# Performance work log

Hardware: AMD Instinct MI355X
Metric: run time of the kernel (lower is better)

Reference implementation:

```python
import jax, jax.numpy as jnp
import numpy as np

EPS = 1e-5  # torch LayerNorm default
NUM_HEADS = 8


def layernorm(x, g, b):
    m = jnp.mean(x, axis=-1, keepdims=True)
    v = jnp.var(x, axis=-1, keepdims=True)
    return (x - m) * jax.lax.rsqrt(v + EPS) * g + b


def dwconv(x_img, w, b):
    # x_img: [B,C,H,W]; w: [C,1,k,k] depthwise, 'same' padding
    C = x_img.shape[1]
    k = w.shape[-1]
    out = jax.lax.conv_general_dilated(
        x_img, w, (1, 1), [(k // 2, k // 2)] * 2,
        dimension_numbers=('NCHW', 'OIHW', 'NCHW'), feature_group_count=C)
    return out + b[None, :, None, None]


def _forward(x, domain_label, cpe_w, cpe_b, ln1_g, ln1_b, qkv_w, proj_w, proj_b,
             dl_w1, dl_b1, dl_w2, dl_b2, crpe_w3, crpe_b3, crpe_w5, crpe_b5,
             crpe_w7, crpe_b7, ln2_g, ln2_b, fc1_w, fc1_b, fc2_w, fc2_b, H, W, d):
    B, N, C = x.shape
    h = NUM_HEADS
    Ch = C // h
    scale = Ch ** (-0.5)

    # ---- CPE: depthwise 3x3 conv positional encoding with residual ----
    xi = x.transpose(0, 2, 1).reshape(B, C, H, W)
    xi = dwconv(xi, cpe_w, cpe_b) + xi
    x = xi.reshape(B, C, N).transpose(0, 2, 1)

    # ---- domain-indexed LayerNorm 1 (d is a static python int) ----
    cur = layernorm(x, ln1_g[d], ln1_b[d])

    # ---- factorized attention ----
    qkv = (cur @ qkv_w).reshape(B, N, 3, h, Ch).transpose(2, 0, 3, 1, 4)
    q, k, v = qkv[0], qkv[1], qkv[2]          # each [B,h,N,Ch]
    k_sm = jax.nn.softmax(k, axis=2)          # softmax over tokens
    kv = jnp.einsum('bhnk,bhnv->bhkv', k_sm, v)       # [B,h,Ch,Ch]
    factor_att = jnp.einsum('bhnk,bhkv->bhnv', q, kv)  # [B,h,N,Ch]

    # ---- conv relative position encoding (window splits {3:2,5:3,7:3}) ----
    v_img = v.transpose(0, 1, 3, 2).reshape(B, C, H, W)
    g1 = dwconv(v_img[:, :2 * Ch], crpe_w3, crpe_b3)
    g2 = dwconv(v_img[:, 2 * Ch:5 * Ch], crpe_w5, crpe_b5)
    g3 = dwconv(v_img[:, 5 * Ch:], crpe_w7, crpe_b7)
    conv_v = jnp.concatenate([g1, g2, g3], axis=1)        # [B,C,H,W]
    conv_v = conv_v.reshape(B, h, Ch, N).transpose(0, 1, 3, 2)
    crpe = q * conv_v                                      # [B,h,N,Ch]

    factor_att = scale * factor_att + crpe

    # ---- per-domain softmax gating over heads ----
    da = jax.nn.relu(domain_label @ dl_w1 + dl_b1) @ dl_w2 + dl_b2  # [B, h*Ch]
    da = da.reshape(B, h, Ch)[:, :, None, :]                        # [B,h,1,Ch]
    da = jax.nn.softmax(da, axis=1)                                  # over heads
    attn = (da * factor_att).transpose(0, 2, 1, 3).reshape(B, N, C)
    attn = attn @ proj_w + proj_b

    x = x + attn

    # ---- domain-indexed LayerNorm 2 + MLP ----
    cur = layernorm(x, ln2_g[d], ln2_b[d])
    cur = jax.nn.gelu(cur @ fc1_w + fc1_b, approximate=False) @ fc2_w + fc2_b
    return x + cur


def setup_inputs() -> dict:
    key = jax.random.key(0)
    ks = iter(jax.random.split(key, 32))
    B, H, W, C, h, nd = 8, 56, 56, 256, 8, 4
    N = H * W
    Ch = C // h
    hid = C // 2   # domain MLP hidden = max(dim//r,4), r=2
    mh = 4 * C     # mlp_ratio=4
    r = lambda shape, s=0.02: jax.random.normal(next(ks), shape, jnp.float32) * s
    return dict(
        x=jax.random.normal(next(ks), (B, N, C), jnp.float32),
        domain_label=jax.nn.one_hot(
            jax.random.randint(next(ks), (B,), 0, nd), nd, dtype=jnp.float32),
        cpe_w=r((C, 1, 3, 3)), cpe_b=jnp.zeros((C,), jnp.float32),
        ln1_g=jnp.ones((nd, C), jnp.float32), ln1_b=jnp.zeros((nd, C), jnp.float32),
        qkv_w=r((C, 3 * C)),
        proj_w=r((C, C)), proj_b=jnp.zeros((C,), jnp.float32),
        dl_w1=r((nd, hid)), dl_b1=jnp.zeros((hid,), jnp.float32),
        dl_w2=r((hid, C)), dl_b2=jnp.zeros((C,), jnp.float32),
        crpe_w3=r((2 * Ch, 1, 3, 3)), crpe_b3=jnp.zeros((2 * Ch,), jnp.float32),
        crpe_w5=r((3 * Ch, 1, 5, 5)), crpe_b5=jnp.zeros((3 * Ch,), jnp.float32),
        crpe_w7=r((3 * Ch, 1, 7, 7)), crpe_b7=jnp.zeros((3 * Ch,), jnp.float32),
        ln2_g=jnp.ones((nd, C), jnp.float32), ln2_b=jnp.zeros((nd, C), jnp.float32),
        fc1_w=r((C, mh)), fc1_b=jnp.zeros((mh,), jnp.float32),
        fc2_w=r((mh, C)), fc2_b=jnp.zeros((C,), jnp.float32),
        H=H, W=W, d=0,
    )


def reference(x, domain_label, cpe_w, cpe_b, ln1_g, ln1_b, qkv_w, proj_w, proj_b,
              dl_w1, dl_b1, dl_w2, dl_b2, crpe_w3, crpe_b3, crpe_w5, crpe_b5,
              crpe_w7, crpe_b7, ln2_g, ln2_b, fc1_w, fc1_b, fc2_w, fc2_b, H, W, d):
    return _forward(x, domain_label, cpe_w, cpe_b, ln1_g, ln1_b, qkv_w, proj_w,
                    proj_b, dl_w1, dl_b1, dl_w2, dl_b2, crpe_w3, crpe_b3, crpe_w5,
                    crpe_b5, crpe_w7, crpe_b7, ln2_g, ln2_b, fc1_w, fc1_b, fc2_w,
                    fc2_b, H, W, d)
```

## Files before the change

### kernel.cpp

```cpp
#include <hip/hip_runtime.h>
#include <hip/hip_bf16.h>
#include <math.h>

#define BB 8
#define HH 56
#define WW 56
#define NN (HH*WW)
#define CC 256
#define NH 8
#define NT (BB*NN)
#define HID 128
#define MH 1024
#define SCALE 0.17677669529663687f

typedef __attribute__((ext_vector_type(8))) short bf16x8;
typedef __attribute__((ext_vector_type(4))) float f32x4;

__device__ __forceinline__ ushort f2bf(float f) {
    __hip_bfloat16 h = __float2bfloat16(f);
    return *(ushort*)&h;
}
__device__ __forceinline__ float bf2f(ushort u) {
    union { unsigned int i; float f; } x; x.i = ((unsigned int)u) << 16; return x.f;
}
__device__ __forceinline__ uint pk2(float lo, float hi) {
    return ((uint)f2bf(hi) << 16) | (uint)f2bf(lo);
}
__device__ __forceinline__ float unlo(uint u) { return __uint_as_float(u << 16); }
__device__ __forceinline__ float unhi(uint u) { return __uint_as_float(u & 0xFFFF0000u); }

__device__ __forceinline__ void gload16(const void* g, void* s) {
    __builtin_amdgcn_global_load_lds(
        (const __attribute__((address_space(1))) void*)g,
        (__attribute__((address_space(3))) void*)s, 16, 0, 0);
}

__global__ __launch_bounds__(256) void wtrans_kernel(
    const float* __restrict__ w, ushort* __restrict__ wt, int K, int N)
{
    __shared__ float tile[32][33];
    const int t = threadIdx.x;
    const int col = t & 31, rw = t >> 5;
    const int k0 = blockIdx.y * 32, n0 = blockIdx.x * 32;
    #pragma unroll
    for (int i = rw; i < 32; i += 8)
        tile[i][col] = w[(size_t)(k0 + i) * N + n0 + col];
    __syncthreads();
    #pragma unroll
    for (int i = rw; i < 32; i += 8) {
        int n = n0 + i;
        int nl = n & 63;
        int np = (n & ~63) | ((nl & 3) * 16 + (nl >> 2));
        wt[(size_t)np * K + k0 + col] = f2bf(tile[col][i]);
    }
}

__global__ __launch_bounds__(256) void wpack_kernel(
    const float* __restrict__ w3, const float* __restrict__ b3,
    const float* __restrict__ w5, const float* __restrict__ b5,
    const float* __restrict__ w7, const float* __restrict__ b7,
    uint* __restrict__ wt, float* __restrict__ bt)
{
    const int qq = blockIdx.x;
    const int KSQ = (qq == 0) ? 3 : (qq == 1) ? 5 : 7;
    for (int idx = threadIdx.x; idx < 49 * 32; idx += 256) {
        int tap = idx >> 5, p = idx & 31;
        int cA = qq * 64 + 2 * p;
        float lo = 0.f, hi = 0.f;
        if (tap < KSQ * KSQ) {
            int dy = tap / KSQ, dx = tap - dy * KSQ;
            const float* wb; int kslo;
            if (cA < 64)       { wb = w3 + cA * 9;          kslo = 3; }
            else if (cA < 160) { wb = w5 + (cA - 64) * 25;  kslo = 5; }
            else               { wb = w7 + (cA - 160) * 49; kslo = 7; }
            int offp = KSQ / 2 - kslo / 2;
            int sy = dy - offp, sx = dx - offp;
            if (sy >= 0 && sy < kslo && sx >= 0 && sx < kslo) {
                lo = wb[sy * kslo + sx];
                hi = wb[kslo * kslo + sy * kslo + sx];
            }
        }
        wt[(qq * 49 + tap) * 32 + p] = pk2(lo, hi);
    }
    if (threadIdx.x < 32) {
        int p = threadIdx.x, cA = qq * 64 + 2 * p;
        float blo, bhi;
        if (cA < 64)       { blo = b3[cA];       bhi = b3[cA + 1]; }
        else if (cA < 160) { blo = b5[cA - 64];  bhi = b5[cA - 63]; }
        else               { blo = b7[cA - 160]; bhi = b7[cA - 159]; }
        bt[(qq * 32 + p) * 2]     = blo;
        bt[(qq * 32 + p) * 2 + 1] = bhi;
    }
}

__global__ __launch_bounds__(256) void cpack_kernel(
    const float* __restrict__ w, const float* __restrict__ bias,
    uint* __restrict__ wt, float* __restrict__ bt)
{
    const int qq = blockIdx.x;
    for (int idx = threadIdx.x; idx < 9 * 32; idx += 256) {
        int tap = idx >> 5, p = idx & 31;
        int cA = qq * 64 + 2 * p;
        wt[(qq * 9 + tap) * 32 + p] = pk2(w[cA * 9 + tap], w[(cA + 1) * 9 + tap]);
    }
    if (threadIdx.x < 32) {
        int p = threadIdx.x, cA = qq * 64 + 2 * p;
        bt[(qq * 32 + p) * 2]     = bias[cA];
        bt[(qq * 32 + p) * 2 + 1] = bias[cA + 1];
    }
}

__global__ __launch_bounds__(256) void cpe_kernel(
    const float* __restrict__ x, const uint* __restrict__ wtab,
    const float* __restrict__ btab, float* __restrict__ out)
{
    __shared__ uint vt[4 * 34 * 32];
    const int qq = blockIdx.x >> 1, hx = blockIdx.x & 1;
    const int y0 = blockIdx.y * 2, b = blockIdx.z;
    const int x0 = hx * 28;
    const int t = threadIdx.x;
    const int c0 = qq * 64;
    const int p = t & 31;

    uint wpk[9];
    #pragma unroll
    for (int i = 0; i < 9; ++i) wpk[i] = wtab[(qq * 9 + i) * 32 + p];
    const float2 bb = *(const float2*)(btab + (qq * 32 + p) * 2);

    for (int pos = t >> 5; pos < 4 * 34; pos += 8) {
        int row = pos / 34, col = pos - row * 34;
        int gy = y0 + row - 1, gx = x0 + col - 3;
        float2 v = {0.f, 0.f};
        if ((unsigned)gy < 56u && (unsigned)gx < 56u)
            v = *(const float2*)(x + ((size_t)b * NN + gy * 56 + gx) * CC + c0 + 2 * p);
        vt[pos * 32 + p] = pk2(v.x, v.y);
    }
    __syncthreads();

    const int rseg = t >> 5;
    const int r = rseg >> 2, sg = rseg & 3;
    float accA[7], accB[7];
    #pragma unroll
    for (int k = 0; k < 7; ++k) { accA[k] = bb.x; accB[k] = bb.y; }

    #pragma unroll
    for (int dy = 0; dy < 3; ++dy) {
        const int rowbase = (r + dy) * 34 * 32;
        float fA[9], fB[9];
        #pragma unroll
        for (int u = 0; u < 9; ++u) {
            uint vv = vt[rowbase + (sg * 7 + 2 + u) * 32 + p];
            fA[u] = unlo(vv); fB[u] = unhi(vv);
        }
        #pragma unroll
        for (int dx = 0; dx < 3; ++dx) {
            uint wv = wpk[dy * 3 + dx];
            float wl = unlo(wv), wh = unhi(wv);
            #pragma unroll
            for (int k = 0; k < 7; ++k) {
                accA[k] = fmaf(fA[dx + k], wl, accA[k]);
                accB[k] = fmaf(fB[dx + k], wh, accB[k]);
            }
        }
    }

    const int cA = c0 + 2 * p;
    const int ytok = y0 + r;
    #pragma unroll
    for (int k = 0; k < 7; ++k) {
        size_t tok = (size_t)b * NN + ytok * 56 + x0 + sg * 7 + k;
        float2 res = *(const float2*)(x + tok * CC + cA);
        float2 o = { accA[k] + res.x, accB[k] + res.y };
        *(float2*)(out + tok * CC + cA) = o;
    }
}

__global__ __launch_bounds__(256) void ln_kernel(
    const float* __restrict__ src, const float* __restrict__ g_all,
    const float* __restrict__ b_all, const int* __restrict__ dptr,
    ushort* __restrict__ dst)
{
    const int wid = threadIdx.x >> 6, lane = threadIdx.x & 63;
    const int row = blockIdx.x * 4 + wid;
    const int d = *dptr;
    const float* g = g_all + d * CC;
    const float* be = b_all + d * CC;
    const float* p = src + (size_t)row * CC;
    float4 v = *(const float4*)(p + lane * 4);
    float s = v.x + v.y + v.z + v.w;
    float sq = v.x*v.x + v.y*v.y + v.z*v.z + v.w*v.w;
    #pragma unroll
    for (int off = 1; off < 64; off <<= 1) {
        s  += __shfl_xor(s, off);
        sq += __shfl_xor(sq, off);
    }
    const float mean = s * (1.f / CC);
    const float var = sq * (1.f / CC) - mean * mean;
    const float rs = rsqrtf(var + 1e-5f);
    float4 g4 = *(const float4*)(g + lane * 4);
    float4 b4 = *(const float4*)(be + lane * 4);
    ushort4 o4;
    o4.x = f2bf((v.x - mean) * rs * g4.x + b4.x);
    o4.y = f2bf((v.y - mean) * rs * g4.y + b4.y);
    o4.z = f2bf((v.z - mean) * rs * g4.z + b4.z);
    o4.w = f2bf((v.w - mean) * rs * g4.w + b4.w);
    *(ushort4*)(dst + (size_t)row * CC + lane * 4) = o4;
}

template<int EPI>
__global__ __launch_bounds__(256) void gemm_mfma(
    const ushort* __restrict__ A, const ushort* __restrict__ Bt,
    const float* __restrict__ bias, const float* __restrict__ res,
    void* __restrict__ Cv, int M, int N, int K, int nbn, int nwg)
{
    __shared__ __align__(16) ushort Als[128 * 32];
    __shared__ __align__(16) ushort Bls[128 * 32];
    const int t = threadIdx.x;
    const int lin = blockIdx.x;
    const int q8 = nwg >> 3, r8 = nwg & 7;
    const int xcd = lin & 7, i8 = lin >> 3;
    const int wgid = (xcd < r8 ? xcd * (q8 + 1) : r8 * (q8 + 1) + (xcd - r8) * q8) + i8;
    const int bm = wgid / nbn, bn = wgid - bm * nbn;
    const int brow = bm * 128, bcol = bn * 128;
    const int lane = t & 63, w = t >> 6;
    const int wr = w >> 1, wc = w & 1;
    const int lrow = lane & 15, lko = (lane >> 4) * 8;

    const ushort* gA0 = A + (size_t)(brow + (t >> 2)) * K + (t & 3) * 8;
    const ushort* gA1 = gA0 + (size_t)64 * K;
    const ushort* gB0 = Bt + (size_t)(bcol + (t >> 2)) * K + (t & 3) * 8;
    const ushort* gB1 = gB0 + (size_t)64 * K;
    ushort* lA0 = &Als[t * 8];  ushort* lA1 = &Als[64 * 32 + t * 8];
    ushort* lB0 = &Bls[t * 8];  ushort* lB1 = &Bls[64 * 32 + t * 8];

    f32x4 acc[4][4] = {};

    for (int kt = 0; kt < K; kt += 32) {
        gload16(gA0 + kt, lA0);
        gload16(gA1 + kt, lA1);
        gload16(gB0 + kt, lB0);
        gload16(gB1 + kt, lB1);
        __syncthreads();
        bf16x8 af[4], bfr[4];
        #pragma unroll
        for (int i = 0; i < 4; ++i)
            af[i] = *(const bf16x8*)&Als[(wr * 64 + i * 16 + lrow) * 32 + lko];
        #pragma unroll
        for (int j = 0; j < 4; ++j)
            bfr[j] = *(const bf16x8*)&Bls[(wc * 64 + j * 16 + lrow) * 32 + lko];
        #pragma unroll
        for (int i = 0; i < 4; ++i)
            #pragma unroll
            for (int j = 0; j < 4; ++j)
                acc[i][j] = __builtin_amdgcn_mfma_f32_16x16x32_bf16(
                    af[i], bfr[j], acc[i][j], 0, 0, 0);
        __syncthreads();
    }

    float* Cf = (float*)Cv;
    ushort* Ch = (ushort*)Cv;
    const int col0 = bcol + wc * 64 + 4 * lrow;
    float bias4[4] = {0.f, 0.f, 0.f, 0.f};
    if (EPI >= 2) {
        float4 bv = *(const float4*)(bias + col0);
        bias4[0] = bv.x; bias4[1] = bv.y; bias4[2] = bv.z; bias4[3] = bv.w;
    }
    #pragma unroll
    for (int i = 0; i < 4; ++i) {
        #pragma unroll
        for (int r = 0; r < 4; ++r) {
            const int row = brow + wr * 64 + i * 16 + (lane >> 4) * 4 + r;
            size_t off = (size_t)row * N + col0;
            float o[4];
            #pragma unroll
            for (int j = 0; j < 4; ++j) o[j] = acc[i][j][r] + bias4[j];
            if (EPI == 2) {
                #pragma unroll
                for (int j = 0; j < 4; ++j)
                    o[j] = 0.5f * o[j] * (1.f + erff(o[j] * 0.70710678118654752f));
                ushort4 st = { f2bf(o[0]), f2bf(o[1]), f2bf(o[2]), f2bf(o[3]) };
                *(ushort4*)(Ch + off) = st;
            } else if (EPI == 1) {
                ushort4 st = { f2bf(o[0]), f2bf(o[1]), f2bf(o[2]), f2bf(o[3]) };
                *(ushort4*)(Ch + off) = st;
            } else {
                float4 rv = *(const float4*)(res + off);
                float4 st = { o[0] + rv.x, o[1] + rv.y, o[2] + rv.z, o[3] + rv.w };
                *(float4*)(Cf + off) = st;
            }
        }
    }
}

__global__ __launch_bounds__(256) void kmax1_kernel(
    const ushort* __restrict__ qkv, float* __restrict__ pmax)
{
    const int chunk = blockIdx.x, b = blockIdx.y, c = threadIdx.x;
    const ushort* kb = qkv + (size_t)(b * NN + chunk * 98) * 768 + 256 + c;
    float m = -3.4e38f;
    for (int i = 0; i < 98; ++i) m = fmaxf(m, bf2f(kb[(size_t)i * 768]));
    pmax[(b * 32 + chunk) * CC + c] = m;
}

__global__ __launch_bounds__(256) void kmax2_kernel(
    const float* __restrict__ pmax, float* __restrict__ cmax)
{
    const int b = blockIdx.x, c = threadIdx.x;
    float m = -3.4e38f;
    #pragma unroll
    for (int i = 0; i < 32; ++i) m = fmaxf(m, pmax[(b * 32 + i) * CC + c]);
    cmax[b * CC + c] = m;
}

__global__ __launch_bounds__(256) void kvacc_kernel(
    const ushort* __restrict__ qkv, const float* __restrict__ cmax,
    float* __restrict__ partial, float* __restrict__ psum)
{
    const int chunk = blockIdx.x, h = blockIdx.y, b = blockIdx.z;
    const int t = threadIdx.x;
    const int ck = t & 31, g = t >> 5;
    const int n0 = chunk * 196;
    const ushort* kb = qkv + (size_t)(b * NN + n0) * 768 + 256 + h * 32 + ck;
    const ushort* vb = qkv + (size_t)(b * NN + n0) * 768 + 512 + h * 32 + g * 4;
    const float cm = cmax[b * CC + h * 32 + ck];
    float a0 = 0.f, a1 = 0.f, a2 = 0.f, a3 = 0.f, s = 0.f;
    for (int i = 0; i < 196; ++i) {
        float e = __expf(bf2f(kb[(size_t)i * 768]) - cm);
        ushort4 v4 = *(const ushort4*)(vb + (size_t)i * 768);
        a0 += e * bf2f(v4.x); a1 += e * bf2f(v4.y);
        a2 += e * bf2f(v4.z); a3 += e * bf2f(v4.w);
        s += e;
    }
    float4 o = {a0, a1, a2, a3};
    *(float4*)(partial + ((((size_t)chunk * 8 + b) * 8 + h) * 32 + ck) * 32 + g * 4) = o;
    if (g == 0) psum[((chunk * 8 + b) * 8 + h) * 32 + ck] = s;
}

__global__ __launch_bounds__(256) void kvnorm_kernel(
    const float* __restrict__ partial, const float* __restrict__ psum,
    float* __restrict__ kv)
{
    const int idx = blockIdx.x * 256 + threadIdx.x;
    const int ckidx = idx >> 5;
    float sum = 0.f, cs = 0.f;
    #pragma unroll
    for (int ch = 0; ch < 16; ++ch) {
        sum += partial[(size_t)ch * 65536 + idx];
        cs  += psum[ch * 2048 + ckidx];
    }
    kv[idx] = sum / cs;
}

__global__ __launch_bounds__(256) void fa_kernel(
    ushort* __restrict__ qkv, const float* __restrict__ kvb)
{
    const int mt = blockIdx.x, h = blockIdx.y, b = blockIdx.z;
    const int t = threadIdx.x;
    const int lane = t & 63, wv = t >> 6;
    const int row0 = mt * 448 + wv * 112;
    const int lr = lane & 15, lk = (lane >> 4) * 8;

    bf16x8 bfr[2];
    #pragma unroll
    for (int jj = 0; jj < 2; ++jj)
        #pragma unroll
        for (int e = 0; e < 8; ++e)
            bfr[jj][e] = (short)f2bf(kvb[((size_t)(b * 8 + h) * 32 + lk + e) * 32 + 2 * lr + jj]);

    #pragma unroll
    for (int i = 0; i < 7; ++i) {
        size_t tok = (size_t)b * NN + row0 + i * 16 + lr;
        bf16x8 af = *(const bf16x8*)(qkv + tok * 768 + h * 32 + lk);
        f32x4 a0 = {0.f, 0.f, 0.f, 0.f}, a1 = {0.f, 0.f, 0.f, 0.f};
        a0 = __builtin_amdgcn_mfma_f32_16x16x32_bf16(af, bfr[0], a0, 0, 0, 0);
        a1 = __builtin_amdgcn_mfma_f32_16x16x32_bf16(af, bfr[1], a1, 0, 0, 0);
        #pragma unroll
        for (int r = 0; r < 4; ++r) {
            size_t trow = (size_t)b * NN + row0 + i * 16 + (lane >> 4) * 4 + r;
            *(uint*)(qkv + trow * 768 + 256 + h * 32 + 2 * lr) = pk2(a0[r], a1[r]);
        }
    }
}

__global__ __launch_bounds__(256) void da_kernel(
    const float* __restrict__ dl, const float* __restrict__ w1,
    const float* __restrict__ b1, const float* __restrict__ w2,
    const float* __restrict__ b2, float* __restrict__ da)
{
    const int b = blockIdx.x, t = threadIdx.x;
    __shared__ float r[HID];
    __shared__ float raw[CC];
    if (t < HID) {
        float s = b1[t];
        #pragma unroll
        for (int k = 0; k < 4; ++k) s += dl[b * 4 + k] * w1[k * HID + t];
        r[t] = fmaxf(s, 0.f);
    }
    __syncthreads();
    float s = b2[t];
    for (int j = 0; j < HID; ++j) s += r[j] * w2[j * CC + t];
    raw[t] = s;
    __syncthreads();
    const int ch = t & 31;
    float m = -3.4e38f;
    #pragma unroll
    for (int hh = 0; hh < NH; ++hh) m = fmaxf(m, raw[hh * 32 + ch]);
    float ssum = 0.f;
    #pragma unroll
    for (int hh = 0; hh < NH; ++hh) ssum += __expf(raw[hh * 32 + ch] - m);
    da[b * CC + t] = __expf(raw[t] - m) / ssum;
}

template<int KS>
__device__ __forceinline__ void comb_body(
    uint* vt, int qq,
    const ushort* __restrict__ qkv, const float* __restrict__ da,
    const uint* __restrict__ wtab, const float* __restrict__ btab,
    ushort* __restrict__ out)
{
    constexpr int R = KS / 2;
    constexpr int TR = KS + 1;
    constexpr int WCOLS = 7 + 2 * R;
    const int hx = blockIdx.x & 1;
    const int y0 = blockIdx.y * 2, b = blockIdx.z;
    const int x0 = hx * 28;
    const int t = threadIdx.x;
    const int c0 = qq * 64;
    const int p = t & 31;

    uint wpk[KS * KS];
    #pragma unroll
    for (int i = 0; i < KS * KS; ++i) wpk[i] = wtab[(qq * 49 + i) * 32 + p];
    const float2 bb = *(const float2*)(btab + (qq * 32 + p) * 2);

    for (int pos = t >> 5; pos < TR * 34; pos += 8) {
        int row = pos / 34, col = pos - row * 34;
        int gy = y0 + row - R, gx = x0 + col - 3;
        uint v = 0;
        if ((unsigned)gy < 56u && (unsigned)gx < 56u)
            v = *(const uint*)(qkv + ((size_t)b * NN + gy * 56 + gx) * 768 + 512 + c0 + 2 * p);
        vt[pos * 32 + p] = v;
    }
    __syncthreads();

    const int rseg = t >> 5;
    const int r = rseg >> 2, sg = rseg & 3;
    float accA[7], accB[7];
    #pragma unroll
    for (int k = 0; k < 7; ++k) { accA[k] = bb.x; accB[k] = bb.y; }

    #pragma unroll
    for (int dy = 0; dy < KS; ++dy) {
        const int rowbase = (r + dy) * 34 * 32;
        float fA[WCOLS], fB[WCOLS];
        #pragma unroll
        for (int u = 0; u < WCOLS; ++u) {
            uint vv = vt[rowbase + (sg * 7 + 3 - R + u) * 32 + p];
            fA[u] = unlo(vv); fB[u] = unhi(vv);
        }
        #pragma unroll
        for (int dx = 0; dx < KS; ++dx) {
            uint wv = wpk[dy * KS + dx];
            float wl = unlo(wv), wh = unhi(wv);
            #pragma unroll
            for (int k = 0; k < 7; ++k) {
                accA[k] = fmaf(fA[dx + k], wl, accA[k]);
                accB[k] = fmaf(fB[dx + k], wh, accB[k]);
            }
        }
    }

    const int cA = c0 + 2 * p;
    const float2 da2 = *(const float2*)(da + b * CC + cA);
    const int ytok = y0 + r;
    #pragma unroll
    for (int k = 0; k < 7; ++k) {
        size_t tok = (size_t)b * NN + ytok * 56 + x0 + sg * 7 + k;
        uint qw = *(const uint*)(qkv + tok * 768 + cA);
        uint fw = *(const uint*)(qkv + tok * 768 + 256 + cA);
        ushort2 o = { f2bf(da2.x * (SCALE * unlo(fw) + unlo(qw) * accA[k])),
                      f2bf(da2.y * (SCALE * unhi(fw) + unhi(qw) * accB[k])) };
        *(ushort2*)(out + tok * CC + cA) = o;
    }
}

__global__ __launch_bounds__(256) void combine_kernel(
    const ushort* __restrict__ qkv, const float* __restrict__ da,
    const uint* __restrict__ wtab, const float* __restrict__ btab,
    ushort* __restrict__ out)
{
    __shared__ uint vt[8 * 34 * 32];
    switch (blockIdx.x >> 1) {
    case 0:  comb_body<3>(vt, 0, qkv, da, wtab, btab, out); break;
    case 1:  comb_body<5>(vt, 1, qkv, da, wtab, btab, out); break;
    case 2:  comb_body<7>(vt, 2, qkv, da, wtab, btab, out); break;
    default: comb_body<7>(vt, 3, qkv, da, wtab, btab, out); break;
    }
}

extern "C" void kernel_launch(void* const* d_in, const int* in_sizes, int n_in,
                              void* d_out, int out_size, void* d_ws, size_t ws_size,
                              hipStream_t stream)
{
    const float* x       = (const float*)d_in[0];
    const float* dlab    = (const float*)d_in[1];
    const float* cpe_w   = (const float*)d_in[2];
    const float* cpe_b   = (const float*)d_in[3];
    const float* ln1_g   = (const float*)d_in[4];
    const float* ln1_b   = (const float*)d_in[5];
    const float* qkv_w   = (const float*)d_in[6];
    const float* proj_w  = (const float*)d_in[7];
    const float* proj_b  = (const float*)d_in[8];
    const float* dl_w1   = (const float*)d_in[9];
    const float* dl_b1   = (const float*)d_in[10];
    const float* dl_w2   = (const float*)d_in[11];
    const float* dl_b2   = (const float*)d_in[12];
    const float* crpe_w3 = (const float*)d_in[13];
    const float* crpe_b3 = (const float*)d_in[14];
    const float* crpe_w5 = (const float*)d_in[15];
    const float* crpe_b5 = (const float*)d_in[16];
    const float* crpe_w7 = (const float*)d_in[17];
    const float* crpe_b7 = (const float*)d_in[18];
    const float* ln2_g   = (const float*)d_in[19];
    const float* ln2_b   = (const float*)d_in[20];
    const float* fc1_w   = (const float*)d_in[21];
    const float* fc1_b   = (const float*)d_in[22];
    const float* fc2_w   = (const float*)d_in[23];
    const float* fc2_b   = (const float*)d_in[24];
    const int*   dptr    = (const int*)d_in[27];

    float* out = (float*)d_out;
    char* W = (char*)d_ws;
    size_t off = 0;
    float* x1 = (float*)(W + off);          off += (size_t)NT * CC * 4;
    ushort* qkvb = (ushort*)(W + off);
    ushort* hidden = (ushort*)(W + off);    off += (size_t)NT * MH * 2;
    ushort* actbf = (ushort*)(W + off);     off += (size_t)NT * CC * 2;
    float* partial = (float*)actbf;
    float* psum = partial + (size_t)16 * 65536;
    float* kvb = (float*)(W + off);         off += (size_t)65536 * 4;
    float* dab = (float*)(W + off);         off += (size_t)BB * CC * 4;
    float* pmax = (float*)(W + off);        off += (size_t)BB * 32 * CC * 4;
    float* cmax = (float*)(W + off);        off += (size_t)BB * CC * 4;
    ushort* wq  = (ushort*)(W + off);       off += (size_t)768 * 256 * 2;
    ushort* wp  = (ushort*)(W + off);       off += (size_t)256 * 256 * 2;
    ushort* w1t = (ushort*)(W + off);       off += (size_t)1024 * 256 * 2;
    ushort* w2t = (ushort*)(W + off);       off += (size_t)256 * 1024 * 2;
    uint* wcomb = (uint*)(W + off);         off += (size_t)4 * 49 * 32 * 4;
    float* bcomb = (float*)(W + off);       off += (size_t)4 * 32 * 2 * 4;
    uint* wcpe = (uint*)(W + off);          off += (size_t)4 * 9 * 32 * 4;
    float* bcpe = (float*)(W + off);        off += (size_t)4 * 32 * 2 * 4;

    hipLaunchKernelGGL(wpack_kernel, dim3(4), dim3(256), 0, stream,
                       crpe_w3, crpe_b3, crpe_w5, crpe_b5, crpe_w7, crpe_b7, wcomb, bcomb);
    hipLaunchKernelGGL(cpack_kernel, dim3(4), dim3(256), 0, stream, cpe_w, cpe_b, wcpe, bcpe);
    hipLaunchKernelGGL(wtrans_kernel, dim3(768 / 32, 256 / 32), dim3(256), 0, stream, qkv_w, wq, 256, 768);
    hipLaunchKernelGGL(wtrans_kernel, dim3(256 / 32, 256 / 32), dim3(256), 0, stream, proj_w, wp, 256, 256);
    hipLaunchKernelGGL(wtrans_kernel, dim3(1024 / 32, 256 / 32), dim3(256), 0, stream, fc1_w, w1t, 256, 1024);
    hipLaunchKernelGGL(wtrans_kernel, dim3(256 / 32, 1024 / 32), dim3(256), 0, stream, fc2_w, w2t, 1024, 256);
    hipLaunchKernelGGL(cpe_kernel, dim3(8, 28, 8), dim3(256), 0, stream, x, wcpe, bcpe, x1);
    hipLaunchKernelGGL(da_kernel, dim3(BB), dim3(256), 0, stream,
                       dlab, dl_w1, dl_b1, dl_w2, dl_b2, dab);
    hipLaunchKernelGGL(ln_kernel, dim3(NT / 4), dim3(256), 0, stream,
                       x1, ln1_g, ln1_b, dptr, actbf);
    hipLaunchKernelGGL(gemm_mfma<1>, dim3(196 * 6), dim3(256), 0, stream,
                       actbf, wq, nullptr, nullptr, (void*)qkvb, NT, 768, 256, 6, 196 * 6);
    hipLaunchKernelGGL(kmax1_kernel, dim3(32, 8), dim3(256), 0, stream, qkvb, pmax);
    hipLaunchKernelGGL(kmax2_kernel, dim3(8), dim3(256), 0, stream, pmax, cmax);
    hipLaunchKernelGGL(kvacc_kernel, dim3(16, 8, 8), dim3(256), 0, stream,
                       qkvb, cmax, partial, psum);
    hipLaunchKernelGGL(kvnorm_kernel, dim3(256), dim3(256), 0, stream,
                       partial, psum, kvb);
    hipLaunchKernelGGL(fa_kernel, dim3(7, 8, 8), dim3(256), 0, stream, qkvb, kvb);
    hipLaunchKernelGGL(combine_kernel, dim3(8, 28, 8), dim3(256), 0, stream,
                       qkvb, dab, wcomb, bcomb, actbf);
    hipLaunchKernelGGL(gemm_mfma<3>, dim3(196 * 2), dim3(256), 0, stream,
                       actbf, wp, proj_b, x1, (void*)out, NT, 256, 256, 2, 196 * 2);
    hipLaunchKernelGGL(ln_kernel, dim3(NT / 4), dim3(256), 0, stream,
                       out, ln2_g, ln2_b, dptr, actbf);
    hipLaunchKernelGGL(gemm_mfma<2>, dim3(196 * 8), dim3(256), 0, stream,
                       actbf, w1t, fc1_b, nullptr, (void*)hidden, NT, 1024, 256, 8, 196 * 8);
    hipLaunchKernelGGL(gemm_mfma<3>, dim3(196 * 2), dim3(256), 0, stream,
                       hidden, w2t, fc2_b, out, (void*)out, NT, 256, 1024, 2, 196 * 2);
}
```

Measured before the change: 396.6 us.

## Double-buffer LDS tiles in MFMA GEMM to overlap global loads with compute

The GEMM kernel now keeps two LDS buffers for the A and B tiles. It issues the global-to-LDS loads for the next K-slice before running the MFMAs on the current one, and drops one of the two barriers per iteration. This hides global load latency behind the matrix math. In exchange it doubles LDS use per block, which may reduce occupancy, and it relies on an explicit vmcnt wait before each barrier.

Result: faster. 386.4 us (-2.6%).

```diff
diff --git a/kernel.cpp b/kernel.cpp
--- a/kernel.cpp
+++ b/kernel.cpp
@@ -213,8 +213,8 @@
     const float* __restrict__ bias, const float* __restrict__ res,
     void* __restrict__ Cv, int M, int N, int K, int nbn, int nwg)
 {
-    __shared__ __align__(16) ushort Als[128 * 32];
-    __shared__ __align__(16) ushort Bls[128 * 32];
+    __shared__ __align__(16) ushort Als[2][128 * 32];
+    __shared__ __align__(16) ushort Bls[2][128 * 32];
     const int t = threadIdx.x;
     const int lin = blockIdx.x;
     const int q8 = nwg >> 3, r8 = nwg & 7;
@@ -230,31 +230,43 @@
     const ushort* gA1 = gA0 + (size_t)64 * K;
     const ushort* gB0 = Bt + (size_t)(bcol + (t >> 2)) * K + (t & 3) * 8;
     const ushort* gB1 = gB0 + (size_t)64 * K;
-    ushort* lA0 = &Als[t * 8];  ushort* lA1 = &Als[64 * 32 + t * 8];
-    ushort* lB0 = &Bls[t * 8];  ushort* lB1 = &Bls[64 * 32 + t * 8];
+    const int dOff = t * 8;
 
     f32x4 acc[4][4] = {};
 
-    for (int kt = 0; kt < K; kt += 32) {
-        gload16(gA0 + kt, lA0);
-        gload16(gA1 + kt, lA1);
-        gload16(gB0 + kt, lB0);
-        gload16(gB1 + kt, lB1);
-        __syncthreads();
+    gload16(gA0, &Als[0][dOff]);
+    gload16(gA1, &Als[0][64 * 32 + dOff]);
+    gload16(gB0, &Bls[0][dOff]);
+    gload16(gB1, &Bls[0][64 * 32 + dOff]);
+    asm volatile("s_waitcnt vmcnt(0)" ::: "memory");
+    __builtin_amdgcn_s_barrier();
+
+    const int KT = K >> 5;
+    int cur = 0;
+    for (int it = 0; it < KT; ++it) {
+        if (it + 1 < KT) {
+            const int ktn = (it + 1) << 5;
+            gload16(gA0 + ktn, &Als[cur ^ 1][dOff]);
+            gload16(gA1 + ktn, &Als[cur ^ 1][64 * 32 + dOff]);
+            gload16(gB0 + ktn, &Bls[cur ^ 1][dOff]);
+            gload16(gB1 + ktn, &Bls[cur ^ 1][64 * 32 + dOff]);
+        }
         bf16x8 af[4], bfr[4];
         #pragma unroll
         for (int i = 0; i < 4; ++i)
-            af[i] = *(const bf16x8*)&Als[(wr * 64 + i * 16 + lrow) * 32 + lko];
+            af[i] = *(const bf16x8*)&Als[cur][(wr * 64 + i * 16 + lrow) * 32 + lko];
         #pragma unroll
         for (int j = 0; j < 4; ++j)
-            bfr[j] = *(const bf16x8*)&Bls[(wc * 64 + j * 16 + lrow) * 32 + lko];
+            bfr[j] = *(const bf16x8*)&Bls[cur][(wc * 64 + j * 16 + lrow) * 32 + lko];
         #pragma unroll
         for (int i = 0; i < 4; ++i)
             #pragma unroll
             for (int j = 0; j < 4; ++j)
                 acc[i][j] = __builtin_amdgcn_mfma_f32_16x16x32_bf16(
                     af[i], bfr[j], acc[i][j], 0, 0, 0);
-        __syncthreads();
+        asm volatile("s_waitcnt vmcnt(0)" ::: "memory");
+        __builtin_amdgcn_s_barrier();
+        cur ^= 1;
     }
 
     float* Cf = (float*)Cv;
```
